# Optimization experiments

Measured on AMD Instinct MI355X. Metric: run time of the kernel, lower is better.

The kernel has to match this reference:

```python
import jax, jax.numpy as jnp
import numpy as np


def setup_inputs() -> dict:
    key = jax.random.key(0)
    ks = jax.random.split(key, 5)
    B, C, hl, wl = 8, 256, 64, 64
    hh, wh = 32, 32
    qd = 64
    return {
        "low_level": jax.random.normal(ks[0], (B, C, hl, wl), dtype=jnp.float32),
        "high_level": jax.random.normal(ks[1], (B, C, hh, wh), dtype=jnp.float32),
        "Wq": jax.random.normal(ks[2], (qd, C), dtype=jnp.float32) * 0.02,
        "bq": jnp.zeros((qd,), dtype=jnp.float32),
        "Wk": jax.random.normal(ks[3], (qd, C), dtype=jnp.float32) * 0.02,
        "bk": jnp.zeros((qd,), dtype=jnp.float32),
        "gamma": jnp.zeros((1,), dtype=jnp.float32),
    }


def reference(low_level, high_level, Wq, bq, Wk, bk, gamma):
    B, C, hl, wl = low_level.shape
    _, _, hh, wh = high_level.shape
    Nl, Nh = hl * wl, hh * wh
    # 1x1 conv projections (conv1x1 == channel matmul)
    # query: [B, Nl, qd]
    q = jnp.einsum("bchw,qc->bhwq", low_level, Wq).reshape(B, Nl, -1) + bq
    # key: [B, qd, Nh]
    k = jnp.einsum("bchw,qc->bqhw", high_level, Wk).reshape(B, -1, Nh) + bk[None, :, None]
    # energy [B, Nl, Nh], softmax over key positions (last dim), no scaling
    energy = jnp.einsum("blq,bqh->blh", q, k)
    attention = jax.nn.softmax(energy, axis=-1)
    # value = raw high_level features; out[b,c,l] = sum_h value[b,c,h] * attention[b,l,h]
    value = high_level.reshape(B, C, Nh)
    out = jnp.einsum("bch,blh->bcl", value, attention).reshape(B, C, hl, wl)
    return gamma[0] * out + low_level
```

## Files before the change

kernel.cpp:

```cpp
#include <hip/hip_runtime.h>
#include <stdint.h>

#define NB   8
#define NC   256
#define NL   4096
#define NH   1024
#define QD   64
#define CH   64
#define NCK  16
#define APAD 40

typedef __attribute__((ext_vector_type(8))) short bf16x8;
typedef __attribute__((ext_vector_type(4))) float f32x4;

typedef const __attribute__((address_space(1))) uint32_t* gp1_t;
typedef __attribute__((address_space(3))) uint32_t* sp3_t;

__device__ __forceinline__ uint32_t f2bf(float f) {
    uint32_t u = __builtin_bit_cast(uint32_t, f);
    return (u + 0x7FFFu + ((u >> 16) & 1u)) >> 16;
}

__device__ __forceinline__ void async16(void* lds, const void* g) {
    __builtin_amdgcn_global_load_lds((gp1_t)g, (sp3_t)lds, 16, 0, 0);
}

union U8 { uint16_t u[8]; bf16x8 v; };

__device__ __forceinline__ bf16x8 pack8(const float* f) {
    U8 t;
#pragma unroll
    for (int i = 0; i < 8; ++i) t.u[i] = (uint16_t)f2bf(f[i]);
    return t.v;
}

__global__ __launch_bounds__(256) void vtrans(const float* __restrict__ high,
                                              uint16_t* __restrict__ vws) {
    int t = blockIdx.x * 256 + threadIdx.x;
    int row = t >> 7;
    int seg = t & 127;
    int b = row >> 8, c = row & 255;
    int h0 = seg << 3;
    const float* src = high + ((size_t)row << 10) + h0;
    float4 a = *(const float4*)src;
    float4 d = *(const float4*)(src + 4);
    uint4 val;
    val.x = f2bf(a.x) | (f2bf(a.y) << 16);
    val.y = f2bf(a.z) | (f2bf(a.w) << 16);
    val.z = f2bf(d.x) | (f2bf(d.y) << 16);
    val.w = f2bf(d.z) | (f2bf(d.w) << 16);
    int ck = h0 >> 6, hl = h0 & 63;
    size_t base = ((size_t)((b * 16 + ck) * 256 + c)) * 128
                + (size_t)(((hl * 2) ^ ((c & 7) << 4)));
    *(uint4*)((char*)vws + base) = val;
}

__global__ __launch_bounds__(256) void kproj(const float* __restrict__ high,
                                             const float* __restrict__ Wk,
                                             const float* __restrict__ bk,
                                             uint16_t* __restrict__ kws) {
    __shared__ uint16_t Alds[64 * APAD];
    int b = blockIdx.x >> 4, hb = blockIdx.x & 15;
    int tid = threadIdx.x;
    int w = tid >> 6, lane = tid & 63;
    int g = lane >> 4, lcol = lane & 15;
    int p = tid >> 4, lg = tid & 15;
    const float* hbase = high + ((size_t)b << 18) + hb * 64;
    f32x4 acc[4];
#pragma unroll
    for (int i = 0; i < 4; ++i) acc[i] = (f32x4){0.f, 0.f, 0.f, 0.f};
    int qd = w * 16 + lcol;

#pragma unroll 1
    for (int cs = 0; cs < 8; ++cs) {
        int c0 = cs * 32;
        const float* r0 = hbase + ((size_t)(c0 + p * 2) << 10) + lg * 4;
        float4 x0 = *(const float4*)r0;
        float4 x1 = *(const float4*)(r0 + 1024);
        const float* wr = Wk + qd * 256 + c0 + g * 8;
        float4 wa = *(const float4*)wr;
        float4 wb = *(const float4*)(wr + 4);
        __syncthreads();
        const float* px0 = (const float*)&x0;
        const float* px1 = (const float*)&x1;
#pragma unroll
        for (int j = 0; j < 4; ++j)
            *(uint32_t*)&Alds[(lg * 4 + j) * APAD + p * 2] =
                f2bf(px0[j]) | (f2bf(px1[j]) << 16);
        __syncthreads();
        float wf[8] = {wa.x, wa.y, wa.z, wa.w, wb.x, wb.y, wb.z, wb.w};
        bf16x8 bfrag = pack8(wf);
#pragma unroll
        for (int mt = 0; mt < 4; ++mt) {
            bf16x8 af = *(const bf16x8*)&Alds[(mt * 16 + lcol) * APAD + g * 8];
            acc[mt] = __builtin_amdgcn_mfma_f32_16x16x32_bf16(af, bfrag, acc[mt], 0, 0, 0);
        }
    }
    float bkv = bk[qd];
    char* kbase = (char*)kws + (size_t)blockIdx.x * 8192;
#pragma unroll
    for (int mt = 0; mt < 4; ++mt)
#pragma unroll
        for (int r = 0; r < 4; ++r) {
            int hl = mt * 16 + g * 4 + r;
            *(uint16_t*)(kbase + hl * 128 + (((qd * 2) ^ ((hl & 7) << 4)))) =
                (uint16_t)f2bf(acc[mt][r] + bkv);
        }
}

__global__ __launch_bounds__(256, 2) void attn(
    const float* __restrict__ low, const float* __restrict__ Wq,
    const float* __restrict__ bq, const float* __restrict__ gamma_p,
    const uint16_t* __restrict__ kws, const uint16_t* __restrict__ vws,
    float* __restrict__ out)
{
    __shared__ char smem[63488];
    char* Kc = smem;
    char* Vc = smem + 8192;
    char* Pl = smem + 40960;
    float* rs = (float*)(smem + 49152);
    uint16_t* Alds = (uint16_t*)(smem + 50176);
    char* Qlds = smem + 55296;

    int blk0 = blockIdx.x;
    int blk = (blk0 & 7) * 64 + (blk0 >> 3);
    int b = blk >> 6;
    int l0 = (blk & 63) * 64;
    int tid = threadIdx.x;
    int w = tid >> 6, lane = tid & 63;
    int g = lane >> 4, lcol = lane & 15;

    const float* lowb = low + ((size_t)b << 20);
    const char* kws_b = (const char*)kws + (size_t)b * 16 * 8192;
    const char* vws_b = (const char*)vws + (size_t)b * 16 * 32768;

#pragma unroll
    for (int r = 0; r < 2; ++r) {
        int off = (r * 4 + w) * 1024;
        async16(Kc + off, kws_b + off + lane * 16);
    }
#pragma unroll
    for (int r = 0; r < 8; ++r) {
        int off = (r * 4 + w) * 1024;
        async16(Vc + off, vws_b + off + lane * 16);
    }

    f32x4 qacc[4];
#pragma unroll
    for (int i = 0; i < 4; ++i) qacc[i] = (f32x4){0.f, 0.f, 0.f, 0.f};
    int p = tid >> 4, lg = tid & 15;
    int qd = w * 16 + lcol;
#pragma unroll 1
    for (int cs = 0; cs < 8; ++cs) {
        int c0 = cs * 32;
        const float* r0 = lowb + ((size_t)(c0 + p * 2) << 12) + l0 + lg * 4;
        float4 x0 = *(const float4*)r0;
        float4 x1 = *(const float4*)(r0 + 4096);
        const float* wr = Wq + qd * 256 + c0 + g * 8;
        float4 wa = *(const float4*)wr;
        float4 wb = *(const float4*)(wr + 4);
        __syncthreads();
        const float* px0 = (const float*)&x0;
        const float* px1 = (const float*)&x1;
#pragma unroll
        for (int j = 0; j < 4; ++j)
            *(uint32_t*)&Alds[(lg * 4 + j) * APAD + p * 2] =
                f2bf(px0[j]) | (f2bf(px1[j]) << 16);
        __syncthreads();
        float wf[8] = {wa.x, wa.y, wa.z, wa.w, wb.x, wb.y, wb.z, wb.w};
        bf16x8 bfrag = pack8(wf);
#pragma unroll
        for (int mt = 0; mt < 4; ++mt) {
            bf16x8 af = *(const bf16x8*)&Alds[(mt * 16 + lcol) * APAD + g * 8];
            qacc[mt] = __builtin_amdgcn_mfma_f32_16x16x32_bf16(af, bfrag, qacc[mt], 0, 0, 0);
        }
    }
    float bqv = bq[qd];
#pragma unroll
    for (int mt = 0; mt < 4; ++mt)
#pragma unroll
        for (int r = 0; r < 4; ++r) {
            int l = mt * 16 + g * 4 + r;
            *(uint16_t*)(Qlds + l * 128 + (((qd * 2) ^ ((l & 7) << 4)))) =
                (uint16_t)f2bf(qacc[mt][r] + bqv);
        }
    __syncthreads();
    bf16x8 qf[4][2];
#pragma unroll
    for (int mt = 0; mt < 4; ++mt)
#pragma unroll
        for (int ks = 0; ks < 2; ++ks) {
            int l = mt * 16 + lcol;
            qf[mt][ks] = *(const bf16x8*)(Qlds + l * 128 +
                          (((ks * 64 + g * 16) ^ ((l & 7) << 4))));
        }

    f32x4 oacc[4][4];
#pragma unroll
    for (int i = 0; i < 4; ++i)
#pragma unroll
        for (int j = 0; j < 4; ++j) oacc[i][j] = (f32x4){0.f, 0.f, 0.f, 0.f};
    float rowp[4][4];
#pragma unroll
    for (int i = 0; i < 4; ++i)
#pragma unroll
        for (int j = 0; j < 4; ++j) rowp[i][j] = 0.f;

    int hrow = w * 16 + lcol;
    int swzh = (hrow & 7) << 4;

#pragma unroll 1
    for (int ck = 0; ck < NCK; ++ck) {
        __syncthreads();

        f32x4 sacc[4];
#pragma unroll
        for (int i = 0; i < 4; ++i) sacc[i] = (f32x4){0.f, 0.f, 0.f, 0.f};
#pragma unroll
        for (int ks = 0; ks < 2; ++ks) {
            bf16x8 kf = *(const bf16x8*)(Kc + hrow * 128 +
                          ((ks * 64 + g * 16) ^ swzh));
#pragma unroll
            for (int mt = 0; mt < 4; ++mt)
                sacc[mt] = __builtin_amdgcn_mfma_f32_16x16x32_bf16(qf[mt][ks], kf, sacc[mt], 0, 0, 0);
        }
#pragma unroll
        for (int mt = 0; mt < 4; ++mt)
#pragma unroll
            for (int r = 0; r < 4; ++r) {
                int l = mt * 16 + g * 4 + r;
                float pv = __expf(sacc[mt][r]);
                rowp[mt][r] += pv;
                *(uint16_t*)(Pl + l * 128 + (((hrow * 2) ^ ((l & 7) << 4)))) =
                    (uint16_t)f2bf(pv);
            }
        __syncthreads();

#pragma unroll
        for (int ks = 0; ks < 2; ++ks) {
            bf16x8 pf[4];
#pragma unroll
            for (int mt = 0; mt < 4; ++mt) {
                int l = mt * 16 + lcol;
                pf[mt] = *(const bf16x8*)(Pl + l * 128 +
                           ((ks * 64 + g * 16) ^ ((l & 7) << 4)));
            }
#pragma unroll
            for (int ct = 0; ct < 4; ++ct) {
                int c = w * 64 + ct * 16 + lcol;
                bf16x8 vf = *(const bf16x8*)(Vc + c * 128 +
                              ((ks * 64 + g * 16) ^ ((c & 7) << 4)));
#pragma unroll
                for (int mt = 0; mt < 4; ++mt)
                    oacc[mt][ct] = __builtin_amdgcn_mfma_f32_16x16x32_bf16(pf[mt], vf, oacc[mt][ct], 0, 0, 0);
            }
        }
        __syncthreads();

        if (ck + 1 < NCK) {
            const char* kg = kws_b + (size_t)(ck + 1) * 8192;
            const char* vg = vws_b + (size_t)(ck + 1) * 32768;
#pragma unroll
            for (int r = 0; r < 2; ++r) {
                int off = (r * 4 + w) * 1024;
                async16(Kc + off, kg + off + lane * 16);
            }
#pragma unroll
            for (int r = 0; r < 8; ++r) {
                int off = (r * 4 + w) * 1024;
                async16(Vc + off, vg + off + lane * 16);
            }
        }
    }

#pragma unroll
    for (int mt = 0; mt < 4; ++mt)
#pragma unroll
        for (int r = 0; r < 4; ++r) {
            float v = rowp[mt][r];
            v += __shfl_xor(v, 1, 64);
            v += __shfl_xor(v, 2, 64);
            v += __shfl_xor(v, 4, 64);
            v += __shfl_xor(v, 8, 64);
            rowp[mt][r] = v;
        }
    if (lcol == 0) {
#pragma unroll
        for (int mt = 0; mt < 4; ++mt)
#pragma unroll
            for (int r = 0; r < 4; ++r)
                rs[w * 64 + mt * 16 + g * 4 + r] = rowp[mt][r];
    }
    __syncthreads();

    float gam = gamma_p[0];
    float inv[4][4];
#pragma unroll
    for (int mt = 0; mt < 4; ++mt)
#pragma unroll
        for (int r = 0; r < 4; ++r) {
            int l = mt * 16 + g * 4 + r;
            inv[mt][r] = gam / (rs[l] + rs[64 + l] + rs[128 + l] + rs[192 + l]);
        }

#pragma unroll
    for (int mt = 0; mt < 4; ++mt) {
        int lbase = l0 + mt * 16 + g * 4;
#pragma unroll
        for (int ct = 0; ct < 4; ++ct) {
            int c = w * 64 + ct * 16 + lcol;
            const float* lp = lowb + ((size_t)c << 12) + lbase;
            float4 lo = *(const float4*)lp;
            float4 res;
            res.x = lo.x + oacc[mt][ct][0] * inv[mt][0];
            res.y = lo.y + oacc[mt][ct][1] * inv[mt][1];
            res.z = lo.z + oacc[mt][ct][2] * inv[mt][2];
            res.w = lo.w + oacc[mt][ct][3] * inv[mt][3];
            *(float4*)(out + (((size_t)(b * 256 + c)) << 12) + lbase) = res;
        }
    }
}

extern "C" void kernel_launch(void* const* d_in, const int* in_sizes, int n_in,
                              void* d_out, int out_size, void* d_ws, size_t ws_size,
                              hipStream_t stream) {
    const float* low   = (const float*)d_in[0];
    const float* high  = (const float*)d_in[1];
    const float* Wq    = (const float*)d_in[2];
    const float* bq    = (const float*)d_in[3];
    const float* Wk    = (const float*)d_in[4];
    const float* bk    = (const float*)d_in[5];
    const float* gamma = (const float*)d_in[6];
    float* out = (float*)d_out;

    uint16_t* kws = (uint16_t*)d_ws;
    uint16_t* vws = (uint16_t*)((char*)d_ws + (1u << 20));

    vtrans<<<dim3(1024), dim3(256), 0, stream>>>(high, vws);
    kproj<<<dim3(128), dim3(256), 0, stream>>>(high, Wk, bk, kws);
    attn<<<dim3(512), dim3(256), 0, stream>>>(low, Wq, bq, gamma, kws, vws, out);
}
```

Baseline: 143.3 us.

## Merge projections into one prep kernel and stream K/V from global into registers

Q projection moves out of the attention kernel into a combined prep kernel that also does the K projection and the V bf16 transpose, so three launches become two. The attention kernel now uses 32-row tiles across 1024 blocks. It reads K and V fragments straight from global memory into registers instead of staging them in LDS with async copies. A double-buffered P tile removes one barrier per chunk. The trade-offs are an extra Q round-trip through global memory, repeated uncached-in-LDS V reads by every block, and unswizzled workspace layouts.

```diff
diff --git a/kernel.cpp b/kernel.cpp
--- a/kernel.cpp
+++ b/kernel.cpp
@@ -1,32 +1,21 @@
 #include <hip/hip_runtime.h>
 #include <stdint.h>
 
-#define NB   8
-#define NC   256
-#define NL   4096
-#define NH   1024
-#define QD   64
-#define CH   64
-#define NCK  16
+
 #define APAD 40
 
 typedef __attribute__((ext_vector_type(8))) short bf16x8;
 typedef __attribute__((ext_vector_type(4))) float f32x4;
-
-typedef const __attribute__((address_space(1))) uint32_t* gp1_t;
-typedef __attribute__((address_space(3))) uint32_t* sp3_t;
 
 __device__ __forceinline__ uint32_t f2bf(float f) {
     uint32_t u = __builtin_bit_cast(uint32_t, f);
     return (u + 0x7FFFu + ((u >> 16) & 1u)) >> 16;
 }
-
-__device__ __forceinline__ void async16(void* lds, const void* g) {
-    __builtin_amdgcn_global_load_lds((gp1_t)g, (sp3_t)lds, 16, 0, 0);
+__device__ __forceinline__ bf16x8 asbf(uint4 v) {
+    return __builtin_bit_cast(bf16x8, v);
 }
 
 union U8 { uint16_t u[8]; bf16x8 v; };
-
 __device__ __forceinline__ bf16x8 pack8(const float* f) {
     U8 t;
 #pragma unroll
@@ -34,50 +23,64 @@
     return t.v;
 }
 
-__global__ __launch_bounds__(256) void vtrans(const float* __restrict__ high,
-                                              uint16_t* __restrict__ vws) {
-    int t = blockIdx.x * 256 + threadIdx.x;
-    int row = t >> 7;
-    int seg = t & 127;
-    int b = row >> 8, c = row & 255;
-    int h0 = seg << 3;
-    const float* src = high + ((size_t)row << 10) + h0;
-    float4 a = *(const float4*)src;
-    float4 d = *(const float4*)(src + 4);
-    uint4 val;
-    val.x = f2bf(a.x) | (f2bf(a.y) << 16);
-    val.y = f2bf(a.z) | (f2bf(a.w) << 16);
-    val.z = f2bf(d.x) | (f2bf(d.y) << 16);
-    val.w = f2bf(d.z) | (f2bf(d.w) << 16);
-    int ck = h0 >> 6, hl = h0 & 63;
-    size_t base = ((size_t)((b * 16 + ck) * 256 + c)) * 128
-                + (size_t)(((hl * 2) ^ ((c & 7) << 4)));
-    *(uint4*)((char*)vws + base) = val;
-}
-
-__global__ __launch_bounds__(256) void kproj(const float* __restrict__ high,
-                                             const float* __restrict__ Wk,
-                                             const float* __restrict__ bk,
-                                             uint16_t* __restrict__ kws) {
+__global__ __launch_bounds__(256) void prep(
+    const float* __restrict__ low, const float* __restrict__ high,
+    const float* __restrict__ Wq, const float* __restrict__ bq,
+    const float* __restrict__ Wk, const float* __restrict__ bk,
+    uint16_t* __restrict__ qws, uint16_t* __restrict__ kws,
+    uint16_t* __restrict__ vws)
+{
     __shared__ uint16_t Alds[64 * APAD];
-    int b = blockIdx.x >> 4, hb = blockIdx.x & 15;
-    int tid = threadIdx.x;
-    int w = tid >> 6, lane = tid & 63;
-    int g = lane >> 4, lcol = lane & 15;
+    int bid = blockIdx.x, tid = threadIdx.x;
+
+    if (bid >= 640) {
+        int v = bid - 640;
+#pragma unroll
+        for (int it = 0; it < 4; ++it) {
+            int t = it * 65536 + v * 256 + tid;
+            int row = t >> 7, seg = t & 127;
+            int b = row >> 8, c = row & 255;
+            int h0 = seg << 3;
+            const float* src = high + ((size_t)row << 10) + h0;
+            float4 a = *(const float4*)src;
+            float4 d = *(const float4*)(src + 4);
+            uint4 val;
+            val.x = f2bf(a.x) | (f2bf(a.y) << 16);
+            val.y = f2bf(a.z) | (f2bf(a.w) << 16);
+            val.z = f2bf(d.x) | (f2bf(d.y) << 16);
+            val.w = f2bf(d.z) | (f2bf(d.w) << 16);
+            int ck = h0 >> 6, hl = h0 & 63;
+            *(uint4*)((char*)vws +
+                ((size_t)((b * 16 + ck) * 256 + c)) * 128 + hl * 2) = val;
+        }
+        return;
+    }
+
+    const float* X; const float* W; const float* bias; uint16_t* dst;
+    int xstride, drow0;
+    if (bid < 512) {
+        int b = bid >> 6, lt = bid & 63;
+        X = low + ((size_t)b << 20) + lt * 64;  xstride = 4096;
+        W = Wq; bias = bq; dst = qws; drow0 = b * 4096 + lt * 64;
+    } else {
+        int r = bid - 512; int b = r >> 4, hb = r & 15;
+        X = high + ((size_t)b << 18) + hb * 64; xstride = 1024;
+        W = Wk; bias = bk; dst = kws; drow0 = b * 1024 + hb * 64;
+    }
+    int w = tid >> 6, lane = tid & 63, g = lane >> 4, lcol = lane & 15;
     int p = tid >> 4, lg = tid & 15;
-    const float* hbase = high + ((size_t)b << 18) + hb * 64;
+    int qd = w * 16 + lcol;
     f32x4 acc[4];
 #pragma unroll
     for (int i = 0; i < 4; ++i) acc[i] = (f32x4){0.f, 0.f, 0.f, 0.f};
-    int qd = w * 16 + lcol;
 
 #pragma unroll 1
     for (int cs = 0; cs < 8; ++cs) {
         int c0 = cs * 32;
-        const float* r0 = hbase + ((size_t)(c0 + p * 2) << 10) + lg * 4;
+        const float* r0 = X + (size_t)(c0 + p * 2) * xstride + lg * 4;
         float4 x0 = *(const float4*)r0;
-        float4 x1 = *(const float4*)(r0 + 1024);
-        const float* wr = Wk + qd * 256 + c0 + g * 8;
+        float4 x1 = *(const float4*)(r0 + xstride);
+        const float* wr = W + qd * 256 + c0 + g * 8;
         float4 wa = *(const float4*)wr;
         float4 wb = *(const float4*)(wr + 4);
         __syncthreads();
@@ -96,185 +99,113 @@
             acc[mt] = __builtin_amdgcn_mfma_f32_16x16x32_bf16(af, bfrag, acc[mt], 0, 0, 0);
         }
     }
-    float bkv = bk[qd];
-    char* kbase = (char*)kws + (size_t)blockIdx.x * 8192;
+    float bv = bias[qd];
 #pragma unroll
     for (int mt = 0; mt < 4; ++mt)
 #pragma unroll
-        for (int r = 0; r < 4; ++r) {
-            int hl = mt * 16 + g * 4 + r;
-            *(uint16_t*)(kbase + hl * 128 + (((qd * 2) ^ ((hl & 7) << 4)))) =
-                (uint16_t)f2bf(acc[mt][r] + bkv);
-        }
-}
-
-__global__ __launch_bounds__(256, 2) void attn(
-    const float* __restrict__ low, const float* __restrict__ Wq,
-    const float* __restrict__ bq, const float* __restrict__ gamma_p,
-    const uint16_t* __restrict__ kws, const uint16_t* __restrict__ vws,
-    float* __restrict__ out)
+        for (int r = 0; r < 4; ++r)
+            dst[(size_t)(drow0 + mt * 16 + g * 4 + r) * 64 + qd] =
+                (uint16_t)f2bf(acc[mt][r] + bv);
+}
+
+__global__ __launch_bounds__(256) void attn(
+    const float* __restrict__ low, const float* __restrict__ gamma_p,
+    const uint16_t* __restrict__ qws, const uint16_t* __restrict__ kws,
+    const uint16_t* __restrict__ vws, float* __restrict__ out)
 {
-    __shared__ char smem[63488];
-    char* Kc = smem;
-    char* Vc = smem + 8192;
-    char* Pl = smem + 40960;
-    float* rs = (float*)(smem + 49152);
-    uint16_t* Alds = (uint16_t*)(smem + 50176);
-    char* Qlds = smem + 55296;
-
-    int blk0 = blockIdx.x;
-    int blk = (blk0 & 7) * 64 + (blk0 >> 3);
-    int b = blk >> 6;
-    int l0 = (blk & 63) * 64;
-    int tid = threadIdx.x;
-    int w = tid >> 6, lane = tid & 63;
+    __shared__ char Pl[8192];
+    __shared__ float rs[128];
+
+    int bid = blockIdx.x;
+    int blk = (bid & 7) * 128 + (bid >> 3);
+    int b = blk >> 7;
+    int l0 = (blk & 127) * 32;
+    int tid = threadIdx.x, w = tid >> 6, lane = tid & 63;
     int g = lane >> 4, lcol = lane & 15;
 
-    const float* lowb = low + ((size_t)b << 20);
-    const char* kws_b = (const char*)kws + (size_t)b * 16 * 8192;
-    const char* vws_b = (const char*)vws + (size_t)b * 16 * 32768;
-
-#pragma unroll
-    for (int r = 0; r < 2; ++r) {
-        int off = (r * 4 + w) * 1024;
-        async16(Kc + off, kws_b + off + lane * 16);
-    }
-#pragma unroll
-    for (int r = 0; r < 8; ++r) {
-        int off = (r * 4 + w) * 1024;
-        async16(Vc + off, vws_b + off + lane * 16);
-    }
-
-    f32x4 qacc[4];
-#pragma unroll
-    for (int i = 0; i < 4; ++i) qacc[i] = (f32x4){0.f, 0.f, 0.f, 0.f};
-    int p = tid >> 4, lg = tid & 15;
-    int qd = w * 16 + lcol;
+    const char* Qb = (const char*)qws + ((size_t)(b * 4096 + l0)) * 128;
+    const char* Kb = (const char*)kws + ((size_t)(b * 1024)) * 128;
+    const char* Vb = (const char*)vws + (size_t)b * 524288;
+
+    bf16x8 qf[2][2];
+#pragma unroll
+    for (int mt = 0; mt < 2; ++mt)
+#pragma unroll
+        for (int ks = 0; ks < 2; ++ks)
+            qf[mt][ks] = asbf(*(const uint4*)(Qb + (mt * 16 + lcol) * 128 + ks * 64 + g * 16));
+
+    int hloc = w * 16 + lcol;
+    uint4 kc0 = *(const uint4*)(Kb + hloc * 128 + g * 16);
+    uint4 kc1 = *(const uint4*)(Kb + hloc * 128 + 64 + g * 16);
+
+    f32x4 oacc[2][4];
+#pragma unroll
+    for (int i = 0; i < 2; ++i)
+#pragma unroll
+        for (int j = 0; j < 4; ++j) oacc[i][j] = (f32x4){0.f, 0.f, 0.f, 0.f};
+    float rowp[2][4];
+#pragma unroll
+    for (int i = 0; i < 2; ++i)
+#pragma unroll
+        for (int j = 0; j < 4; ++j) rowp[i][j] = 0.f;
+
 #pragma unroll 1
-    for (int cs = 0; cs < 8; ++cs) {
-        int c0 = cs * 32;
-        const float* r0 = lowb + ((size_t)(c0 + p * 2) << 12) + l0 + lg * 4;
-        float4 x0 = *(const float4*)r0;
-        float4 x1 = *(const float4*)(r0 + 4096);
-        const float* wr = Wq + qd * 256 + c0 + g * 8;
-        float4 wa = *(const float4*)wr;
-        float4 wb = *(const float4*)(wr + 4);
-        __syncthreads();
-        const float* px0 = (const float*)&x0;
-        const float* px1 = (const float*)&x1;
-#pragma unroll
-        for (int j = 0; j < 4; ++j)
-            *(uint32_t*)&Alds[(lg * 4 + j) * APAD + p * 2] =
-                f2bf(px0[j]) | (f2bf(px1[j]) << 16);
-        __syncthreads();
-        float wf[8] = {wa.x, wa.y, wa.z, wa.w, wb.x, wb.y, wb.z, wb.w};
-        bf16x8 bfrag = pack8(wf);
-#pragma unroll
-        for (int mt = 0; mt < 4; ++mt) {
-            bf16x8 af = *(const bf16x8*)&Alds[(mt * 16 + lcol) * APAD + g * 8];
-            qacc[mt] = __builtin_amdgcn_mfma_f32_16x16x32_bf16(af, bfrag, qacc[mt], 0, 0, 0);
-        }
-    }
-    float bqv = bq[qd];
-#pragma unroll
-    for (int mt = 0; mt < 4; ++mt)
-#pragma unroll
-        for (int r = 0; r < 4; ++r) {
-            int l = mt * 16 + g * 4 + r;
-            *(uint16_t*)(Qlds + l * 128 + (((qd * 2) ^ ((l & 7) << 4)))) =
-                (uint16_t)f2bf(qacc[mt][r] + bqv);
-        }
-    __syncthreads();
-    bf16x8 qf[4][2];
-#pragma unroll
-    for (int mt = 0; mt < 4; ++mt)
-#pragma unroll
-        for (int ks = 0; ks < 2; ++ks) {
-            int l = mt * 16 + lcol;
-            qf[mt][ks] = *(const bf16x8*)(Qlds + l * 128 +
-                          (((ks * 64 + g * 16) ^ ((l & 7) << 4))));
-        }
-
-    f32x4 oacc[4][4];
-#pragma unroll
-    for (int i = 0; i < 4; ++i)
-#pragma unroll
-        for (int j = 0; j < 4; ++j) oacc[i][j] = (f32x4){0.f, 0.f, 0.f, 0.f};
-    float rowp[4][4];
-#pragma unroll
-    for (int i = 0; i < 4; ++i)
-#pragma unroll
-        for (int j = 0; j < 4; ++j) rowp[i][j] = 0.f;
-
-    int hrow = w * 16 + lcol;
-    int swzh = (hrow & 7) << 4;
-
-#pragma unroll 1
-    for (int ck = 0; ck < NCK; ++ck) {
-        __syncthreads();
-
-        f32x4 sacc[4];
-#pragma unroll
-        for (int i = 0; i < 4; ++i) sacc[i] = (f32x4){0.f, 0.f, 0.f, 0.f};
-#pragma unroll
-        for (int ks = 0; ks < 2; ++ks) {
-            bf16x8 kf = *(const bf16x8*)(Kc + hrow * 128 +
-                          ((ks * 64 + g * 16) ^ swzh));
-#pragma unroll
-            for (int mt = 0; mt < 4; ++mt)
-                sacc[mt] = __builtin_amdgcn_mfma_f32_16x16x32_bf16(qf[mt][ks], kf, sacc[mt], 0, 0, 0);
-        }
-#pragma unroll
-        for (int mt = 0; mt < 4; ++mt)
+    for (int ck = 0; ck < 16; ++ck) {
+        char* Pb = Pl + ((ck & 1) << 12);
+        uint4 vf[8];
+#pragma unroll
+        for (int ks = 0; ks < 2; ++ks)
+#pragma unroll
+            for (int ct = 0; ct < 4; ++ct)
+                vf[ks * 4 + ct] = *(const uint4*)(Vb + ck * 32768 +
+                    (w * 64 + ct * 16 + lcol) * 128 + ks * 64 + g * 16);
+
+        f32x4 sacc[2];
+#pragma unroll
+        for (int i = 0; i < 2; ++i) sacc[i] = (f32x4){0.f, 0.f, 0.f, 0.f};
+#pragma unroll
+        for (int mt = 0; mt < 2; ++mt) {
+            sacc[mt] = __builtin_amdgcn_mfma_f32_16x16x32_bf16(qf[mt][0], asbf(kc0), sacc[mt], 0, 0, 0);
+            sacc[mt] = __builtin_amdgcn_mfma_f32_16x16x32_bf16(qf[mt][1], asbf(kc1), sacc[mt], 0, 0, 0);
+        }
+        int nk = ((ck + 1) & 15) * 64 + hloc;
+        uint4 kn0 = *(const uint4*)(Kb + nk * 128 + g * 16);
+        uint4 kn1 = *(const uint4*)(Kb + nk * 128 + 64 + g * 16);
+
+#pragma unroll
+        for (int mt = 0; mt < 2; ++mt)
 #pragma unroll
             for (int r = 0; r < 4; ++r) {
                 int l = mt * 16 + g * 4 + r;
                 float pv = __expf(sacc[mt][r]);
                 rowp[mt][r] += pv;
-                *(uint16_t*)(Pl + l * 128 + (((hrow * 2) ^ ((l & 7) << 4)))) =
+                *(uint16_t*)(Pb + l * 128 + ((hloc * 2) ^ ((l & 7) << 4))) =
                     (uint16_t)f2bf(pv);
             }
         __syncthreads();
 
 #pragma unroll
         for (int ks = 0; ks < 2; ++ks) {
-            bf16x8 pf[4];
-#pragma unroll
-            for (int mt = 0; mt < 4; ++mt) {
+            bf16x8 pf[2];
+#pragma unroll
+            for (int mt = 0; mt < 2; ++mt) {
                 int l = mt * 16 + lcol;
-                pf[mt] = *(const bf16x8*)(Pl + l * 128 +
-                           ((ks * 64 + g * 16) ^ ((l & 7) << 4)));
+                pf[mt] = *(const bf16x8*)(Pb + l * 128 +
+                          ((ks * 64 + g * 16) ^ ((l & 7) << 4)));
             }
 #pragma unroll
             for (int ct = 0; ct < 4; ++ct) {
-                int c = w * 64 + ct * 16 + lcol;
-                bf16x8 vf = *(const bf16x8*)(Vc + c * 128 +
-                              ((ks * 64 + g * 16) ^ ((c & 7) << 4)));
-#pragma unroll
-                for (int mt = 0; mt < 4; ++mt)
-                    oacc[mt][ct] = __builtin_amdgcn_mfma_f32_16x16x32_bf16(pf[mt], vf, oacc[mt][ct], 0, 0, 0);
+                bf16x8 vv = asbf(vf[ks * 4 + ct]);
+#pragma unroll
+                for (int mt = 0; mt < 2; ++mt)
+                    oacc[mt][ct] = __builtin_amdgcn_mfma_f32_16x16x32_bf16(pf[mt], vv, oacc[mt][ct], 0, 0, 0);
             }
         }
-        __syncthreads();
-
-        if (ck + 1 < NCK) {
-            const char* kg = kws_b + (size_t)(ck + 1) * 8192;
-            const char* vg = vws_b + (size_t)(ck + 1) * 32768;
-#pragma unroll
-            for (int r = 0; r < 2; ++r) {
-                int off = (r * 4 + w) * 1024;
-                async16(Kc + off, kg + off + lane * 16);
-            }
-#pragma unroll
-            for (int r = 0; r < 8; ++r) {
-                int off = (r * 4 + w) * 1024;
-                async16(Vc + off, vg + off + lane * 16);
-            }
-        }
-    }
-
-#pragma unroll
-    for (int mt = 0; mt < 4; ++mt)
+        kc0 = kn0; kc1 = kn1;
+    }
+
+#pragma unroll
+    for (int mt = 0; mt < 2; ++mt)
 #pragma unroll
         for (int r = 0; r < 4; ++r) {
             float v = rowp[mt][r];
@@ -286,39 +217,37 @@
         }
     if (lcol == 0) {
 #pragma unroll
-        for (int mt = 0; mt < 4; ++mt)
+        for (int mt = 0; mt < 2; ++mt)
 #pragma unroll
             for (int r = 0; r < 4; ++r)
-                rs[w * 64 + mt * 16 + g * 4 + r] = rowp[mt][r];
+                rs[w * 32 + mt * 16 + g * 4 + r] = rowp[mt][r];
     }
     __syncthreads();
 
     float gam = gamma_p[0];
-    float inv[4][4];
-#pragma unroll
-    for (int mt = 0; mt < 4; ++mt)
+    float inv[2][4];
+#pragma unroll
+    for (int mt = 0; mt < 2; ++mt)
 #pragma unroll
         for (int r = 0; r < 4; ++r) {
             int l = mt * 16 + g * 4 + r;
-            inv[mt][r] = gam / (rs[l] + rs[64 + l] + rs[128 + l] + rs[192 + l]);
-        }
-
-#pragma unroll
-    for (int mt = 0; mt < 4; ++mt) {
-        int lbase = l0 + mt * 16 + g * 4;
+            inv[mt][r] = gam / (rs[l] + rs[32 + l] + rs[64 + l] + rs[96 + l]);
+        }
+
+#pragma unroll
+    for (int mt = 0; mt < 2; ++mt)
 #pragma unroll
         for (int ct = 0; ct < 4; ++ct) {
             int c = w * 64 + ct * 16 + lcol;
-            const float* lp = lowb + ((size_t)c << 12) + lbase;
-            float4 lo = *(const float4*)lp;
+            size_t base = ((size_t)(b * 256 + c) << 12) + l0 + mt * 16 + g * 4;
+            float4 lo = *(const float4*)(low + base);
             float4 res;
             res.x = lo.x + oacc[mt][ct][0] * inv[mt][0];
             res.y = lo.y + oacc[mt][ct][1] * inv[mt][1];
             res.z = lo.z + oacc[mt][ct][2] * inv[mt][2];
             res.w = lo.w + oacc[mt][ct][3] * inv[mt][3];
-            *(float4*)(out + (((size_t)(b * 256 + c)) << 12) + lbase) = res;
-        }
-    }
+            *(float4*)(out + base) = res;
+        }
 }
 
 extern "C" void kernel_launch(void* const* d_in, const int* in_sizes, int n_in,
@@ -333,10 +262,10 @@
     const float* gamma = (const float*)d_in[6];
     float* out = (float*)d_out;
 
-    uint16_t* kws = (uint16_t*)d_ws;
-    uint16_t* vws = (uint16_t*)((char*)d_ws + (1u << 20));
-
-    vtrans<<<dim3(1024), dim3(256), 0, stream>>>(high, vws);
-    kproj<<<dim3(128), dim3(256), 0, stream>>>(high, Wk, bk, kws);
-    attn<<<dim3(512), dim3(256), 0, stream>>>(low, Wq, bq, gamma, kws, vws, out);
-}
+    uint16_t* qws = (uint16_t*)d_ws;
+    uint16_t* kws = (uint16_t*)((char*)d_ws + (4u << 20));
+    uint16_t* vws = (uint16_t*)((char*)d_ws + (5u << 20));
+
+    prep<<<dim3(896), dim3(256), 0, stream>>>(low, high, Wq, bq, Wk, bk, qws, kws, vws);
+    attn<<<dim3(1024), dim3(256), 0, stream>>>(low, gamma, qws, kws, vws, out);
+}
```

Result: slower. 183.7 us (+28.2%).
